# Kernel tuning notes

Hardware: AMD Instinct MI355X
Metric: run time of the kernel (lower is better)

## Reference

```python
import jax, jax.numpy as jnp
import numpy as np

B, S, H = 32, 256, 128
K, C, DSUB, O = 8, 4096, 16, 6  # PQ subspaces, ncentroids=4096, subvector dim, bits/symbol


def setup_inputs() -> dict:
    key = jax.random.key(0)
    ks = jax.random.split(key, 8)
    return {
        "z": jax.random.normal(ks[0], (B, S, 3), jnp.float32),
        "W1": jax.random.normal(ks[1], (3, H), jnp.float32) * 0.3,
        "b1": jax.random.normal(ks[2], (H,), jnp.float32) * 0.1,
        "W2": jax.random.normal(ks[3], (H, H), jnp.float32) * 0.1,
        "b2": jax.random.normal(ks[4], (H,), jnp.float32) * 0.1,
        "centroids": jax.random.normal(ks[5], (K, C, DSUB), jnp.float32),
        "W3": jax.random.normal(ks[6], (H, O), jnp.float32) * 0.1,
        "b3": jax.random.normal(ks[7], (O,), jnp.float32) * 0.1,
    }


def reference(z, W1, b1, W2, b2, centroids, W3, b3):
    # Small demapper MLP (layers 1-2, exact dense math)
    h1 = jax.nn.relu(z @ W1 + b1)            # [B,S,H]
    h2 = jax.nn.relu(h1 @ W2 + b2)           # [B,S,H] == layer3in
    N = B * S
    x = h2.reshape(N, K, DSUB)               # split rows into K PQ subvectors
    # Encode: nearest centroid per subspace (||x-c||^2 argmin; ||x||^2 is constant per row)
    dots = jnp.einsum("nkd,kcd->nkc", x, centroids)      # [N,K,C]
    c_norm = jnp.sum(centroids * centroids, axis=-1)      # [K,C]
    codes = jnp.argmin(c_norm[None, :, :] - 2.0 * dots, axis=-1)  # [N,K] int
    # LUT: precomputed centroid @ W3 per subspace
    W3r = W3.reshape(K, DSUB, O)
    lut = jnp.einsum("kcd,kdo->kco", centroids, W3r)      # [K,C,O]
    # Approximate matmul: sum of LUT entries selected by codes
    approx = jnp.sum(lut[jnp.arange(K)[None, :], codes], axis=1)  # [N,O]
    llr = (approx + b3).reshape(B, S * O)                 # [B, n]
    return llr
```

## Files before the change

kernel.cpp:

```cpp
#include <hip/hip_runtime.h>
#include <hip/hip_fp16.h>
#include <stdint.h>

#define NROWS 8192
#define HDIM  128
#define KSUB  8
#define NC    4096
#define DSUB  16
#define OUTD  6

#define FB_TAU 1.2e-4f
#define DOTSCALE (-2.0f / 4096.0f)
#define QSCALE   (-2048.0f)

typedef _Float16 f16x8 __attribute__((ext_vector_type(8)));
typedef float    f32x4 __attribute__((ext_vector_type(4)));

#define XK_OFF 0u
#define CN_OFF 4194304u
#define B1_OFF 4325376u
#define PK_OFF 6422528u

__global__ __launch_bounds__(256) void prep_kernel(
    const float* __restrict__ z, const float* __restrict__ W1, const float* __restrict__ b1,
    const float* __restrict__ W2, const float* __restrict__ b2,
    const float* __restrict__ ce,
    float* __restrict__ xk, float* __restrict__ cnorm, f16x8* __restrict__ B1S)
{
    __shared__ float h1s[16 * HDIM];
    __shared__ float w2s[HDIM * HDIM];
    const int t = threadIdx.x;
    const int row0 = blockIdx.x * 16;

    {
        const int e = blockIdx.x * 256 + t;
        const int k    = e >> 14;
        const int tile = (e >> 6) & 255;
        const int lane = e & 63;
        const int col  = lane & 15;
        const int quad = lane >> 4;
        const int dims = (quad & 1) * 8;
        const int part = quad >> 1;
        const int n = tile * 16 + col;
        const float* cp = &ce[((size_t)k * NC + n) * DSUB + dims];
        f16x8 hi, lo;
        #pragma unroll
        for (int j = 0; j < 8; ++j) {
            const float s = cp[j] * 16.0f;
            const _Float16 h = (_Float16)s;
            hi[j] = h;
            lo[j] = (_Float16)(s - (float)h);
        }
        B1S[e] = part ? lo : hi;
    }

    if (blockIdx.x < (KSUB * NC) / 256) {
        const int g = blockIdx.x * 256 + t;
        const float4* cp = (const float4*)&ce[(size_t)g * DSUB];
        float nn = 0.f;
        #pragma unroll
        for (int q = 0; q < 4; ++q) {
            const float4 v = cp[q];
            nn = fmaf(v.x, v.x, nn); nn = fmaf(v.y, v.y, nn);
            nn = fmaf(v.z, v.z, nn); nn = fmaf(v.w, v.w, nn);
        }
        cnorm[g] = nn;
    }

    {
        const float4* g4 = (const float4*)W2;
        float4* s4 = (float4*)w2s;
        #pragma unroll
        for (int q = 0; q < 16; ++q) s4[t + q * 256] = g4[t + q * 256];
    }

    #pragma unroll
    for (int e = 0; e < 8; ++e) {
        const int idx = e * 256 + t;
        const int r = idx >> 7, j = idx & 127;
        const int n = row0 + r;
        float acc = b1[j];
        acc = fmaf(z[n * 3 + 0], W1[0 * HDIM + j], acc);
        acc = fmaf(z[n * 3 + 1], W1[1 * HDIM + j], acc);
        acc = fmaf(z[n * 3 + 2], W1[2 * HDIM + j], acc);
        h1s[idx] = fmaxf(acc, 0.f);
    }
    __syncthreads();

    const int c4 = (t & 31) * 4;
    const int r2 = (t >> 5) * 2;
    float acc[2][4];
    #pragma unroll
    for (int a = 0; a < 2; ++a)
        #pragma unroll
        for (int b = 0; b < 4; ++b) acc[a][b] = 0.f;

    for (int k4 = 0; k4 < HDIM; k4 += 4) {
        float hh[2][4], ww[4][4];
        #pragma unroll
        for (int q = 0; q < 2; ++q) {
            const float4 v = *(const float4*)&h1s[(r2 + q) * HDIM + k4];
            hh[q][0] = v.x; hh[q][1] = v.y; hh[q][2] = v.z; hh[q][3] = v.w;
        }
        #pragma unroll
        for (int p = 0; p < 4; ++p) {
            const float4 v = *(const float4*)&w2s[(k4 + p) * HDIM + c4];
            ww[p][0] = v.x; ww[p][1] = v.y; ww[p][2] = v.z; ww[p][3] = v.w;
        }
        #pragma unroll
        for (int q = 0; q < 2; ++q)
            #pragma unroll
            for (int p = 0; p < 4; ++p) {
                acc[q][0] = fmaf(hh[q][p], ww[p][0], acc[q][0]);
                acc[q][1] = fmaf(hh[q][p], ww[p][1], acc[q][1]);
                acc[q][2] = fmaf(hh[q][p], ww[p][2], acc[q][2]);
                acc[q][3] = fmaf(hh[q][p], ww[p][3], acc[q][3]);
            }
    }

    const float4 bb = *(const float4*)&b2[c4];
    const int kk = c4 >> 4;
    const int dd = c4 & 15;
    #pragma unroll
    for (int q = 0; q < 2; ++q) {
        float4 o;
        o.x = fmaxf(acc[q][0] + bb.x, 0.f);
        o.y = fmaxf(acc[q][1] + bb.y, 0.f);
        o.z = fmaxf(acc[q][2] + bb.z, 0.f);
        o.w = fmaxf(acc[q][3] + bb.w, 0.f);
        *(float4*)&xk[((size_t)kk * NROWS + (row0 + r2 + q)) * DSUB + dd] = o;
    }
}

__global__ __launch_bounds__(256, 4) void argmin_kernel(
    const float* __restrict__ xk, const f16x8* __restrict__ B1S,
    const float* __restrict__ cnorm, unsigned long long* __restrict__ pk)
{
    __shared__ float cnL[1024];
    const int t = threadIdx.x;
    const int lane = t & 63;
    const int wid  = t >> 6;
    const int k  = blockIdx.y;
    const int cz = blockIdx.z;
    const int col  = lane & 15;
    const int quad = lane >> 4;
    const int dims = (quad & 1) * 8;
    const int part = quad >> 1;
    const int lane2 = lane ^ 32;
    const int rowbase = (blockIdx.x * 4 + wid) * 64;

    {
        const float* cnp0 = &cnorm[k * NC + cz * 1024];
        #pragma unroll
        for (int q = 0; q < 4; ++q) cnL[t + q * 256] = cnp0[t + q * 256] * QSCALE;
    }

    f16x8 A[4];
    #pragma unroll
    for (int g = 0; g < 4; ++g) {
        const int row = rowbase + g * 16 + col;
        const float* xp = &xk[((size_t)k * NROWS + row) * DSUB + dims];
        f16x8 hi, lo;
        #pragma unroll
        for (int j = 0; j < 8; ++j) {
            const float s = xp[j] * 256.0f;
            const _Float16 h = (_Float16)s;
            hi[j] = h;
            lo[j] = (_Float16)(s - (float)h);
        }
        A[g] = part ? lo : hi;
    }

    float m1[4][4], m2[4][4];
    int   idx[4][4];
    #pragma unroll
    for (int g = 0; g < 4; ++g)
        #pragma unroll
        for (int j = 0; j < 4; ++j) { m1[g][j] = -1e30f; m2[g][j] = -1e30f; idx[g][j] = 0; }

    const f16x8* gp = &B1S[((size_t)k * 256 + cz * 64) * 64];

    f16x8 b1 = gp[lane];
    f16x8 b2 = gp[lane2];

    __syncthreads();

    for (int t64 = 0; t64 < 64; ++t64) {
        const int nt = (t64 + 1) & 63;
        f16x8 nb1 = gp[nt * 64 + lane];
        f16x8 nb2 = gp[nt * 64 + lane2];

        const float nrm = cnL[t64 * 16 + col];
        const f32x4 ci = {nrm, nrm, nrm, nrm};
        const int c = ((cz * 64 + t64) << 4) + col;

        #pragma unroll
        for (int g = 0; g < 4; ++g) {
            f32x4 p = __builtin_amdgcn_mfma_f32_16x16x32_f16(A[g], b1, ci, 0, 0, 0);
            p       = __builtin_amdgcn_mfma_f32_16x16x32_f16(A[g], b2, p, 0, 0, 0);
            #pragma unroll
            for (int j = 0; j < 4; ++j) {
                const float q = p[j];
                const bool gt = q > m1[g][j];
                m2[g][j] = __builtin_amdgcn_fmed3f(q, m1[g][j], m2[g][j]);
                idx[g][j] = gt ? c : idx[g][j];
                m1[g][j] = fmaxf(q, m1[g][j]);
            }
        }
        b1 = nb1;
        b2 = nb2;
    }

    #pragma unroll
    for (int off = 1; off < 16; off <<= 1) {
        #pragma unroll
        for (int g = 0; g < 4; ++g)
            #pragma unroll
            for (int j = 0; j < 4; ++j) {
                const float om1 = __shfl_xor(m1[g][j], off, 64);
                const float om2 = __shfl_xor(m2[g][j], off, 64);
                const int  oidx = __shfl_xor(idx[g][j], off, 64);
                const bool better = (om1 > m1[g][j]) ||
                                    (om1 == m1[g][j] && oidx < idx[g][j]);
                m2[g][j] = fmaxf(fminf(m1[g][j], om1), fmaxf(m2[g][j], om2));
                m1[g][j] = better ? om1 : m1[g][j];
                idx[g][j] = better ? oidx : idx[g][j];
            }
    }

    if (col == 0) {
        #pragma unroll
        for (int g = 0; g < 4; ++g)
            #pragma unroll
            for (int j = 0; j < 4; ++j) {
                const int row = rowbase + g * 16 + quad * 4 + j;
                const float s1 = m1[g][j] * DOTSCALE;
                const float dl = (m1[g][j] - m2[g][j]) * (2.0f / 4096.0f);
                unsigned u = __float_as_uint(s1);
                u = (u & 0x80000000u) ? ~u : (u | 0x80000000u);
                const unsigned short dh = __half_as_ushort(__float2half(dl));
                pk[((size_t)cz * NROWS + row) * KSUB + k] =
                    ((unsigned long long)u << 32) |
                    ((unsigned)dh << 16) | (unsigned)idx[g][j];
            }
    }
}

__global__ __launch_bounds__(256) void finish_kernel(
    const float* __restrict__ xk, const float* __restrict__ ce,
    const float* __restrict__ cnorm, const unsigned long long* __restrict__ pk,
    const float* __restrict__ W3, const float* __restrict__ b3,
    float* __restrict__ out)
{
    __shared__ int codes_s[256];
    __shared__ int wl_s[256];
    __shared__ int wcnt;
    const int t = threadIdx.x;
    const int row0 = blockIdx.x * 32;
    if (t == 0) wcnt = 0;
    __syncthreads();

    {
        const int row = row0 + (t >> 3);
        const int k = t & 7;
        unsigned long long p[4];
        #pragma unroll
        for (int s = 0; s < 4; ++s)
            p[s] = pk[((size_t)s * NROWS + row) * KSUB + k];
        unsigned long long w = p[0];
        #pragma unroll
        for (int s = 1; s < 4; ++s) w = p[s] < w ? p[s] : w;
        const unsigned uw = (unsigned)(w >> 32);
        const float m1w = __uint_as_float((uw & 0x80000000u) ? (uw ^ 0x80000000u) : ~uw);
        float m2g = m1w + (float)__ushort_as_half((unsigned short)((unsigned)w >> 16));
        #pragma unroll
        for (int s = 0; s < 4; ++s) {
            if (p[s] != w) {
                const unsigned us = (unsigned)(p[s] >> 32);
                m2g = fminf(m2g, __uint_as_float(
                    (us & 0x80000000u) ? (us ^ 0x80000000u) : ~us));
            }
        }
        codes_s[t] = (int)(w & 0xFFFFull);
        if (m2g - m1w < FB_TAU) {
            const int slot = atomicAdd(&wcnt, 1);
            wl_s[slot] = t;
        }
    }
    __syncthreads();

    {
        const int lane = t & 63;
        const int wid = t >> 6;
        const int nitems = wcnt;
        for (int i = wid; i < nitems; i += 4) {
            const int wg = wl_s[i];
            const int row = row0 + (wg >> 3), k = wg & 7;
            float xr[DSUB];
            {
                const float* xp = &xk[((size_t)k * NROWS + row) * DSUB];
                #pragma unroll
                for (int q = 0; q < DSUB; q += 4) {
                    const float4 v = *(const float4*)&xp[q];
                    xr[q + 0] = -2.f * v.x; xr[q + 1] = -2.f * v.y;
                    xr[q + 2] = -2.f * v.z; xr[q + 3] = -2.f * v.w;
                }
            }
            float bm = 1e30f; int bi = NC;
            for (int c = lane; c < NC; c += 64) {
                const float* cp = &ce[((size_t)k * NC + c) * DSUB];
                float s = cnorm[k * NC + c];
                #pragma unroll
                for (int d = 0; d < DSUB; ++d) s = fmaf(xr[d], cp[d], s);
                if (s < bm) { bm = s; bi = c; }
            }
            #pragma unroll
            for (int off = 1; off < 64; off <<= 1) {
                const float om = __shfl_xor(bm, off, 64);
                const int  oi = __shfl_xor(bi, off, 64);
                const bool better = (om < bm) || (om == bm && oi < bi);
                bm = better ? om : bm;
                bi = better ? oi : bi;
            }
            if (lane == 0) codes_s[wg] = bi;
        }
    }
    __syncthreads();

    if (t < 32 * OUTD) {
        const int nl = t / OUTD;
        const int o = t - nl * OUTD;
        const int n = row0 + nl;
        float acc = b3[o];
        #pragma unroll
        for (int k = 0; k < KSUB; ++k) {
            const int code = codes_s[nl * KSUB + k];
            const float* cp = &ce[((size_t)k * NC + code) * DSUB];
            const float* wp = &W3[(k * DSUB) * OUTD + o];
            #pragma unroll
            for (int d = 0; d < DSUB; ++d)
                acc = fmaf(cp[d], wp[d * OUTD], acc);
        }
        out[n * OUTD + o] = acc;
    }
}

extern "C" void kernel_launch(void* const* d_in, const int* in_sizes, int n_in,
                              void* d_out, int out_size, void* d_ws, size_t ws_size,
                              hipStream_t stream)
{
    const float* z  = (const float*)d_in[0];
    const float* W1 = (const float*)d_in[1];
    const float* b1 = (const float*)d_in[2];
    const float* W2 = (const float*)d_in[3];
    const float* b2 = (const float*)d_in[4];
    const float* ce = (const float*)d_in[5];
    const float* W3 = (const float*)d_in[6];
    const float* b3 = (const float*)d_in[7];

    char* ws = (char*)d_ws;
    float* xk    = (float*)(ws + XK_OFF);
    float* cnorm = (float*)(ws + CN_OFF);
    f16x8* B1S   = (f16x8*)(ws + B1_OFF);
    unsigned long long* pk = (unsigned long long*)(ws + PK_OFF);

    hipLaunchKernelGGL(prep_kernel, dim3(512), dim3(256), 0, stream,
                       z, W1, b1, W2, b2, ce, xk, cnorm, B1S);
    hipLaunchKernelGGL(argmin_kernel, dim3(32, 8, 4), dim3(256), 0, stream,
                       xk, B1S, cnorm, pk);
    hipLaunchKernelGGL(finish_kernel, dim3(256), dim3(256), 0, stream,
                       xk, ce, cnorm, pk, W3, b3, (float*)d_out);
}
```

Baseline: 177.2 us.

## Stage centroid tiles into LDS via async global_load_lds double buffering

The argmin kernel now copies centroid fp16 tiles into a double-buffered LDS array with global_load_lds, so the next chunk loads while the current one is computed. Before, each lane read its B operand straight from global memory. Each wave now handles 32 rows instead of 64 and the grid grows to 2048 blocks, flattened and remapped so that blocks sharing a subspace are grouped, with a higher occupancy hint. The aim is to hide global latency and improve L2 locality, at the cost of more blocks, per-chunk barriers and less B reuse per wave.

```diff
diff --git a/kernel.cpp b/kernel.cpp
--- a/kernel.cpp
+++ b/kernel.cpp
@@ -20,6 +20,12 @@
 #define CN_OFF 4194304u
 #define B1_OFF 4325376u
 #define PK_OFF 6422528u
+
+__device__ __forceinline__ void stage16(const char* g, char* l) {
+    __builtin_amdgcn_global_load_lds(
+        (const __attribute__((address_space(1))) char*)g,
+        (__attribute__((address_space(3))) char*)l, 16, 0, 0);
+}
 
 __global__ __launch_bounds__(256) void prep_kernel(
     const float* __restrict__ z, const float* __restrict__ W1, const float* __restrict__ b1,
@@ -132,33 +138,42 @@
     }
 }
 
-__global__ __launch_bounds__(256, 4) void argmin_kernel(
+__global__ __launch_bounds__(256, 6) void argmin_kernel(
     const float* __restrict__ xk, const f16x8* __restrict__ B1S,
     const float* __restrict__ cnorm, unsigned long long* __restrict__ pk)
 {
-    __shared__ float cnL[1024];
+    __shared__ f16x8 cs[2][512];
     const int t = threadIdx.x;
     const int lane = t & 63;
     const int wid  = t >> 6;
-    const int k  = blockIdx.y;
-    const int cz = blockIdx.z;
+    const int f = blockIdx.x;
+    const int orig = (f & 7) * 256 + (f >> 3);
+    const int bx = orig & 63;
+    const int k  = (orig >> 6) & 7;
+    const int cz = orig >> 9;
     const int col  = lane & 15;
     const int quad = lane >> 4;
     const int dims = (quad & 1) * 8;
     const int part = quad >> 1;
     const int lane2 = lane ^ 32;
-    const int rowbase = (blockIdx.x * 4 + wid) * 64;
-
-    {
-        const float* cnp0 = &cnorm[k * NC + cz * 1024];
-        #pragma unroll
-        for (int q = 0; q < 4; ++q) cnL[t + q * 256] = cnp0[t + q * 256] * QSCALE;
-    }
-
-    f16x8 A[4];
-    #pragma unroll
-    for (int g = 0; g < 4; ++g) {
-        const int row = rowbase + g * 16 + col;
+    const int rb = bx * 4 + wid;
+
+    const char* gsrc = (const char*)&B1S[((size_t)k * 256 + cz * 64) * 64];
+    const float* cnp = &cnorm[k * NC + cz * 1024];
+
+    #define STAGE(ch_, b_) do {                                                  \
+        const char* s_ = gsrc + (ch_) * 8192 + wid * 2048 + lane * 16;           \
+        char* d_ = (char*)&cs[b_][0] + wid * 2048;                               \
+        stage16(s_,        d_);                                                  \
+        stage16(s_ + 1024, d_ + 1024);                                           \
+    } while (0)
+
+    STAGE(0, 0);
+
+    f16x8 A[2];
+    #pragma unroll
+    for (int g = 0; g < 2; ++g) {
+        const int row = rb * 32 + g * 16 + col;
         const float* xp = &xk[((size_t)k * NROWS + row) * DSUB + dims];
         f16x8 hi, lo;
         #pragma unroll
@@ -171,50 +186,51 @@
         A[g] = part ? lo : hi;
     }
 
-    float m1[4][4], m2[4][4];
-    int   idx[4][4];
-    #pragma unroll
-    for (int g = 0; g < 4; ++g)
+    float m1[2][4], m2[2][4];
+    int   idx[2][4];
+    #pragma unroll
+    for (int g = 0; g < 2; ++g)
         #pragma unroll
         for (int j = 0; j < 4; ++j) { m1[g][j] = -1e30f; m2[g][j] = -1e30f; idx[g][j] = 0; }
 
-    const f16x8* gp = &B1S[((size_t)k * 256 + cz * 64) * 64];
-
-    f16x8 b1 = gp[lane];
-    f16x8 b2 = gp[lane2];
-
-    __syncthreads();
-
-    for (int t64 = 0; t64 < 64; ++t64) {
-        const int nt = (t64 + 1) & 63;
-        f16x8 nb1 = gp[nt * 64 + lane];
-        f16x8 nb2 = gp[nt * 64 + lane2];
-
-        const float nrm = cnL[t64 * 16 + col];
-        const f32x4 ci = {nrm, nrm, nrm, nrm};
-        const int c = ((cz * 64 + t64) << 4) + col;
-
-        #pragma unroll
-        for (int g = 0; g < 4; ++g) {
-            f32x4 p = __builtin_amdgcn_mfma_f32_16x16x32_f16(A[g], b1, ci, 0, 0, 0);
-            p       = __builtin_amdgcn_mfma_f32_16x16x32_f16(A[g], b2, p, 0, 0, 0);
-            #pragma unroll
-            for (int j = 0; j < 4; ++j) {
-                const float q = p[j];
-                const bool gt = q > m1[g][j];
-                m2[g][j] = __builtin_amdgcn_fmed3f(q, m1[g][j], m2[g][j]);
-                idx[g][j] = gt ? c : idx[g][j];
-                m1[g][j] = fmaxf(q, m1[g][j]);
-            }
-        }
-        b1 = nb1;
-        b2 = nb2;
-    }
+    __syncthreads();
+
+    for (int ch = 0; ch < 8; ++ch) {
+        const int cur = ch & 1;
+        float nr[8];
+        #pragma unroll
+        for (int tt = 0; tt < 8; ++tt) nr[tt] = cnp[(ch * 8 + tt) * 16 + col];
+        if (ch < 7) STAGE(ch + 1, cur ^ 1);
+
+        #pragma unroll
+        for (int tt = 0; tt < 8; ++tt) {
+            const f16x8 b1 = cs[cur][tt * 64 + lane];
+            const f16x8 b2 = cs[cur][tt * 64 + lane2];
+            const float nq = nr[tt] * QSCALE;
+            const f32x4 ci = {nq, nq, nq, nq};
+            const int c = ((cz * 64 + ch * 8 + tt) << 4) + col;
+            #pragma unroll
+            for (int g = 0; g < 2; ++g) {
+                f32x4 p = __builtin_amdgcn_mfma_f32_16x16x32_f16(A[g], b1, ci, 0, 0, 0);
+                p       = __builtin_amdgcn_mfma_f32_16x16x32_f16(A[g], b2, p, 0, 0, 0);
+                #pragma unroll
+                for (int j = 0; j < 4; ++j) {
+                    const float q = p[j];
+                    const bool gt = q > m1[g][j];
+                    m2[g][j] = __builtin_amdgcn_fmed3f(q, m1[g][j], m2[g][j]);
+                    idx[g][j] = gt ? c : idx[g][j];
+                    m1[g][j] = fmaxf(q, m1[g][j]);
+                }
+            }
+        }
+        if (ch < 7) __syncthreads();
+    }
+    #undef STAGE
 
     #pragma unroll
     for (int off = 1; off < 16; off <<= 1) {
         #pragma unroll
-        for (int g = 0; g < 4; ++g)
+        for (int g = 0; g < 2; ++g)
             #pragma unroll
             for (int j = 0; j < 4; ++j) {
                 const float om1 = __shfl_xor(m1[g][j], off, 64);
@@ -230,10 +246,10 @@
 
     if (col == 0) {
         #pragma unroll
-        for (int g = 0; g < 4; ++g)
+        for (int g = 0; g < 2; ++g)
             #pragma unroll
             for (int j = 0; j < 4; ++j) {
-                const int row = rowbase + g * 16 + quad * 4 + j;
+                const int row = rb * 32 + g * 16 + quad * 4 + j;
                 const float s1 = m1[g][j] * DOTSCALE;
                 const float dl = (m1[g][j] - m2[g][j]) * (2.0f / 4096.0f);
                 unsigned u = __float_as_uint(s1);
@@ -366,7 +382,7 @@
 
     hipLaunchKernelGGL(prep_kernel, dim3(512), dim3(256), 0, stream,
                        z, W1, b1, W2, b2, ce, xk, cnorm, B1S);
-    hipLaunchKernelGGL(argmin_kernel, dim3(32, 8, 4), dim3(256), 0, stream,
+    hipLaunchKernelGGL(argmin_kernel, dim3(2048), dim3(256), 0, stream,
                        xk, B1S, cnorm, pk);
     hipLaunchKernelGGL(finish_kernel, dim3(256), dim3(256), 0, stream,
                        xk, ce, cnorm, pk, W3, b3, (float*)d_out);
```

Measured after the change: 182.3 us. +2.9%, slower.
